# Kernel optimization log

Measured on AMD Instinct MI355X. Metric: run time of the kernel, lower is better.

The kernel has to match this reference:

```python
import jax, jax.numpy as jnp
import numpy as np

T = 16384
D_IN = 512
D_HID = 512
D_OUT = 512


def setup_inputs() -> dict:
    key = jax.random.key(0)
    ks = jax.random.split(key, 7)
    s_in = 1.0 / np.sqrt(D_IN)
    s_hid = 1.0 / np.sqrt(D_HID)
    xs = jax.random.normal(ks[0], (T, D_IN), dtype=jnp.float32)
    Wz = jax.random.uniform(ks[1], (D_HID, D_IN), jnp.float32, -s_in, s_in)
    bz = jax.random.uniform(ks[2], (D_HID,), jnp.float32, -s_in, s_in)
    Wh = jax.random.uniform(ks[3], (D_HID, D_IN), jnp.float32, -s_in, s_in)
    bh = jax.random.uniform(ks[4], (D_HID,), jnp.float32, -s_in, s_in)
    Wo = jax.random.uniform(ks[5], (D_OUT, D_HID), jnp.float32, -s_hid, s_hid)
    bo = jax.random.uniform(ks[6], (D_OUT,), jnp.float32, -s_hid, s_hid)
    return {"xs": xs, "Wz": Wz, "bz": bz, "Wh": Wh, "bh": bh, "Wo": Wo, "bo": bo}


def _combine(first, second):
    a0, b0 = first
    a1, b1 = second
    return (a0 * a1, a1 * b0 + b1)


def reference(xs, Wz, bz, Wh, bh, Wo, bo):
    # gates and candidate hidden states: [T, H]
    zs = jax.nn.sigmoid(xs @ Wz.T + bz)
    hs = xs @ Wh.T + bh
    # prepend identity element (a=1, b=0) for the h_0 = 0 initial state
    a = jnp.concatenate([jnp.ones((1, zs.shape[1]), zs.dtype), 1.0 - zs], axis=0)
    b = jnp.concatenate([jnp.zeros((1, zs.shape[1]), zs.dtype), zs * hs], axis=0)
    _, states = jax.lax.associative_scan(_combine, (a, b))  # [T+1, H]
    return states[1:] @ Wo.T + bo  # [T, D_OUT]
```

## Files before the change

kernel.cpp:

```cpp
#include <hip/hip_runtime.h>
#include <hip/hip_bf16.h>
#include <cstdint>
#include <cmath>

#define T_SEQ 16384
#define DMODEL 512
#define NCHUNK 512
#define LCHUNK 32
#define W_N    (DMODEL * DMODEL)
#define N4_W   (W_N / 4)
#define N4_W3  (3 * N4_W)
#define N4_X   (T_SEQ * DMODEL / 4)
#define N4_ALL (N4_W3 + N4_X)
#define NTILE  8

typedef __bf16 bf16x8 __attribute__((ext_vector_type(8)));
typedef float  f32x4  __attribute__((ext_vector_type(4)));

using bf16 = __hip_bfloat16;

__device__ __forceinline__ void load_lds16(const void* g, void* l) {
    __builtin_amdgcn_global_load_lds((const __attribute__((address_space(1))) void*)g,
                                     (__attribute__((address_space(3))) void*)l,
                                     16, 0, 0);
}

__device__ __forceinline__ unsigned short f2bf(float f) {
    union { float f; unsigned u; } v; v.f = f;
    const unsigned r = (v.u + 0x7FFFu + ((v.u >> 16) & 1u)) >> 16;
    return (unsigned short)r;
}
__device__ __forceinline__ float bf2f(unsigned short u) {
    union { unsigned u; float f; } v; v.u = ((unsigned)u) << 16;
    return v.f;
}

__device__ __forceinline__ void comb(float& A, float& B, float fA, float fB,
                                     float sA, float sB) {
    A = fA * sA;
    B = sA * fB + sB;
}

__global__ __launch_bounds__(256) void k_convert(
    const float* __restrict__ xs,
    const float* __restrict__ Wz, const float* __restrict__ Wh,
    const float* __restrict__ Wo,
    bf16* __restrict__ xs_c, bf16* __restrict__ Wz_c,
    bf16* __restrict__ Wh_c, bf16* __restrict__ Wo_c)
{
    const int i = blockIdx.x * 256 + threadIdx.x;
    if (i >= N4_ALL) return;
    const float* src; bf16* dst; int o;
    if (i < N4_W3) {
        const int w = i >> 16; o = i & 65535;
        src = (w == 0) ? Wz : (w == 1) ? Wh : Wo;
        dst = (w == 0) ? Wz_c : (w == 1) ? Wh_c : Wo_c;
    } else {
        o = i - N4_W3; src = xs; dst = xs_c;
    }
    const float4 v = ((const float4*)src)[o];
    ushort4 r;
    r.x = f2bf(v.x); r.y = f2bf(v.y); r.z = f2bf(v.z); r.w = f2bf(v.w);
    ((ushort4*)dst)[o] = r;
}

__global__ __launch_bounds__(512, 2) void gemm_zh(
    const bf16* __restrict__ xs_c, const bf16* __restrict__ Wz, const float* __restrict__ bz,
    const bf16* __restrict__ Wh, const float* __restrict__ bh,
    unsigned int* __restrict__ ab_ws,
    float* __restrict__ AaggT, float* __restrict__ BaggT)
{
    __shared__ __bf16 As[2][2][256 * 32];
    __shared__ __bf16 Zs[2][2][128 * 32];
    __shared__ __bf16 Hs[2][2][128 * 32];

    const int tid  = threadIdx.x;
    const int bm   = blockIdx.x;
    const int bn   = blockIdx.y;
    const int lane = tid & 63;
    const int wave = tid >> 6;
    const int wm   = wave >> 1;
    const int wn   = wave & 1;
    const int quad = lane >> 4;
    const int col  = lane & 15;

    f32x4 accz[4][4], acch[4][4];
    #pragma unroll
    for (int i = 0; i < 4; ++i)
        #pragma unroll
        for (int j = 0; j < 4; ++j) {
            accz[i][j] = (f32x4){0.f, 0.f, 0.f, 0.f};
            acch[i][j] = (f32x4){0.f, 0.f, 0.f, 0.f};
        }

    const int srow = tid >> 2;
    const int wq   = (tid & 3) ^ ((tid >> 3) & 3);
    const bf16* ag = xs_c + (size_t)(bm * 256 + srow) * DMODEL + wq * 8;
    const bf16* zg = Wz   + (size_t)(bn * 128 + srow) * DMODEL + wq * 8;
    const bf16* hg = Wh   + (size_t)(bn * 128 + srow) * DMODEL + wq * 8;

    const int fq = quad ^ ((col >> 1) & 3);
    int offA[4], offB[4];
    #pragma unroll
    for (int i = 0; i < 4; ++i) {
        offA[i] = (wm * 64 + i * 16 + col) * 32 + fq * 8;
        offB[i] = (wn * 64 + i * 16 + col) * 32 + fq * 8;
    }

    auto STAGE_HALF = [&](int t, int h) {
        const int b  = t & 1;
        const int ko = t * 64 + h * 32;
        load_lds16(ag + ko,                          &As[b][h][tid * 8]);
        load_lds16(ag + (size_t)128 * DMODEL + ko,   &As[b][h][(512 + tid) * 8]);
        load_lds16(zg + ko,                          &Zs[b][h][tid * 8]);
        load_lds16(hg + ko,                          &Hs[b][h][tid * 8]);
    };

    STAGE_HALF(0, 0); STAGE_HALF(0, 1);

    #pragma unroll
    for (int t = 0; t < NTILE; ++t) {
        const int b = t & 1;
        bf16x8 af[4], zf[4], hf[4];

        asm volatile("s_waitcnt vmcnt(4)" ::: "memory");
        __builtin_amdgcn_s_barrier();
        __builtin_amdgcn_sched_barrier(0);
        if (t + 1 < NTILE) STAGE_HALF(t + 1, 0);
        #pragma unroll
        for (int i = 0; i < 4; ++i) {
            af[i] = *(const bf16x8*)&As[b][0][offA[i]];
            zf[i] = *(const bf16x8*)&Zs[b][0][offB[i]];
        }
        __builtin_amdgcn_s_setprio(1);
        #pragma unroll
        for (int i = 0; i < 4; ++i)
            #pragma unroll
            for (int j = 0; j < 4; ++j)
                accz[i][j] = __builtin_amdgcn_mfma_f32_16x16x32_bf16(af[i], zf[j], accz[i][j], 0, 0, 0);
        __builtin_amdgcn_s_setprio(0);

        #pragma unroll
        for (int j = 0; j < 4; ++j)
            hf[j] = *(const bf16x8*)&Hs[b][0][offB[j]];
        __builtin_amdgcn_s_setprio(1);
        #pragma unroll
        for (int i = 0; i < 4; ++i)
            #pragma unroll
            for (int j = 0; j < 4; ++j)
                acch[i][j] = __builtin_amdgcn_mfma_f32_16x16x32_bf16(af[i], hf[j], acch[i][j], 0, 0, 0);
        __builtin_amdgcn_s_setprio(0);

        if (t + 1 < NTILE) {
            asm volatile("s_waitcnt vmcnt(4)" ::: "memory");
        } else {
            asm volatile("s_waitcnt vmcnt(0)" ::: "memory");
        }
        __builtin_amdgcn_s_barrier();
        __builtin_amdgcn_sched_barrier(0);
        if (t + 1 < NTILE) STAGE_HALF(t + 1, 1);
        #pragma unroll
        for (int i = 0; i < 4; ++i) {
            af[i] = *(const bf16x8*)&As[b][1][offA[i]];
            zf[i] = *(const bf16x8*)&Zs[b][1][offB[i]];
        }
        __builtin_amdgcn_s_setprio(1);
        #pragma unroll
        for (int i = 0; i < 4; ++i)
            #pragma unroll
            for (int j = 0; j < 4; ++j)
                accz[i][j] = __builtin_amdgcn_mfma_f32_16x16x32_bf16(af[i], zf[j], accz[i][j], 0, 0, 0);
        __builtin_amdgcn_s_setprio(0);

        #pragma unroll
        for (int j = 0; j < 4; ++j)
            hf[j] = *(const bf16x8*)&Hs[b][1][offB[j]];
        __builtin_amdgcn_s_setprio(1);
        #pragma unroll
        for (int i = 0; i < 4; ++i)
            #pragma unroll
            for (int j = 0; j < 4; ++j)
                acch[i][j] = __builtin_amdgcn_mfma_f32_16x16x32_bf16(af[i], hf[j], acch[i][j], 0, 0, 0);
        __builtin_amdgcn_s_setprio(0);
    }

    const int c_lo = bm * 8 + wm * 2;
    #pragma unroll
    for (int j = 0; j < 4; ++j) {
        const int n = bn * 128 + wn * 64 + j * 16 + col;
        const float bzv = bz[n];
        const float bhv = bh[n];
        float cA[4], cB[4];
        #pragma unroll
        for (int i = 0; i < 4; ++i) {
            const int mbase = bm * 256 + wm * 64 + i * 16 + quad * 4;
            float A = 1.f, B = 0.f;
            #pragma unroll
            for (int r = 0; r < 4; ++r) {
                const float zpre = accz[i][j][r] + bzv;
                const float hpre = acch[i][j][r] + bhv;
                const float z = 1.f / (1.f + __expf(-zpre));
                const float a = 1.f - z;
                const float b = z * hpre;
                const size_t idx = (size_t)(mbase + r) * DMODEL + n;
                ab_ws[idx] = (unsigned)f2bf(a) | ((unsigned)f2bf(b) << 16);
                A = a * A;
                B = a * B + b;
            }
            cA[i] = A; cB[i] = B;
        }
        #pragma unroll
        for (int i = 0; i < 4; ++i) {
            float pA = __shfl_xor(cA[i], 16);
            float pB = __shfl_xor(cB[i], 16);
            const bool hi1 = quad & 1;
            comb(cA[i], cB[i], hi1 ? pA : cA[i], hi1 ? pB : cB[i],
                               hi1 ? cA[i] : pA, hi1 ? cB[i] : pB);
            pA = __shfl_xor(cA[i], 32);
            pB = __shfl_xor(cB[i], 32);
            const bool hi2 = quad >> 1;
            comb(cA[i], cB[i], hi2 ? pA : cA[i], hi2 ? pB : cB[i],
                               hi2 ? cA[i] : pA, hi2 ? cB[i] : pB);
        }
        float Alo, Blo, Ahi, Bhi;
        comb(Alo, Blo, cA[0], cB[0], cA[1], cB[1]);
        comb(Ahi, Bhi, cA[2], cB[2], cA[3], cB[3]);
        if (quad == 0) {
            AaggT[(size_t)n * NCHUNK + c_lo]     = Alo;
            BaggT[(size_t)n * NCHUNK + c_lo]     = Blo;
            AaggT[(size_t)n * NCHUNK + c_lo + 1] = Ahi;
            BaggT[(size_t)n * NCHUNK + c_lo + 1] = Bhi;
        }
    }
}

__global__ __launch_bounds__(512) void scan_p2(
    const float* __restrict__ AaggT, const float* __restrict__ BaggT,
    float* __restrict__ HpreT)
{
    const int h = blockIdx.x;
    const int c = threadIdx.x;
    __shared__ float sA[NCHUNK], sB[NCHUNK];

    float A = AaggT[(size_t)h * NCHUNK + c];
    float B = BaggT[(size_t)h * NCHUNK + c];
    sA[c] = A; sB[c] = B;
    __syncthreads();

    for (int off = 1; off < NCHUNK; off <<= 1) {
        float pA = 1.f, pB = 0.f;
        if (c >= off) { pA = sA[c - off]; pB = sB[c - off]; }
        __syncthreads();
        const float nB = A * pB + B;
        const float nA = A * pA;
        A = nA; B = nB;
        sA[c] = A; sB[c] = B;
        __syncthreads();
    }
    const float hp = (c == 0) ? 0.f : sB[c - 1];
    HpreT[(size_t)h * NCHUNK + c] = hp;
}

__global__ __launch_bounds__(256) void scan_p3(
    const unsigned int* __restrict__ ab_ws, const float* __restrict__ HpreT,
    unsigned short* __restrict__ states)
{
    const int tid = threadIdx.x;
    const int c   = blockIdx.x;
    const int ch  = blockIdx.y * 256 + tid;
    float H = HpreT[(size_t)ch * NCHUNK + c];
    const size_t base = (size_t)(c * LCHUNK) * DMODEL + ch;
    #pragma unroll 8
    for (int i = 0; i < LCHUNK; ++i) {
        const unsigned u = ab_ws[base + (size_t)i * DMODEL];
        const float a = bf2f((unsigned short)(u & 0xFFFFu));
        const float b = bf2f((unsigned short)(u >> 16));
        H = a * H + b;
        states[base + (size_t)i * DMODEL] = f2bf(H);
    }
}

__global__ __launch_bounds__(512, 2) void gemm_out(
    const bf16* __restrict__ states, const bf16* __restrict__ Wo, const float* __restrict__ bo,
    float* __restrict__ out)
{
    __shared__ __bf16 As[2][2][256 * 32];
    __shared__ __bf16 Bs[2][2][128 * 32];

    const int tid  = threadIdx.x;
    const int bm   = blockIdx.x;
    const int bn   = blockIdx.y;
    const int lane = tid & 63;
    const int wave = tid >> 6;
    const int wm   = wave >> 1;
    const int wn   = wave & 1;
    const int quad = lane >> 4;
    const int col  = lane & 15;

    f32x4 acc[4][4];
    #pragma unroll
    for (int i = 0; i < 4; ++i)
        #pragma unroll
        for (int j = 0; j < 4; ++j)
            acc[i][j] = (f32x4){0.f, 0.f, 0.f, 0.f};

    const int srow = tid >> 2;
    const int wq   = (tid & 3) ^ ((tid >> 3) & 3);
    const bf16* ag = states + (size_t)(bm * 256 + srow) * DMODEL + wq * 8;
    const bf16* bg = Wo     + (size_t)(bn * 128 + srow) * DMODEL + wq * 8;

    const int fq = quad ^ ((col >> 1) & 3);
    int offA[4], offB[4];
    #pragma unroll
    for (int i = 0; i < 4; ++i) {
        offA[i] = (wm * 64 + i * 16 + col) * 32 + fq * 8;
        offB[i] = (wn * 64 + i * 16 + col) * 32 + fq * 8;
    }

    auto STAGE_HALF = [&](int t, int h) {
        const int b  = t & 1;
        const int ko = t * 64 + h * 32;
        load_lds16(ag + ko,                        &As[b][h][tid * 8]);
        load_lds16(ag + (size_t)128 * DMODEL + ko, &As[b][h][(512 + tid) * 8]);
        load_lds16(bg + ko,                        &Bs[b][h][tid * 8]);
    };

    STAGE_HALF(0, 0); STAGE_HALF(0, 1);

    #pragma unroll
    for (int t = 0; t < NTILE; ++t) {
        const int b = t & 1;
        bf16x8 af[4], bf[4];

        asm volatile("s_waitcnt vmcnt(3)" ::: "memory");
        __builtin_amdgcn_s_barrier();
        __builtin_amdgcn_sched_barrier(0);
        if (t + 1 < NTILE) STAGE_HALF(t + 1, 0);
        #pragma unroll
        for (int i = 0; i < 4; ++i) {
            af[i] = *(const bf16x8*)&As[b][0][offA[i]];
            bf[i] = *(const bf16x8*)&Bs[b][0][offB[i]];
        }
        __builtin_amdgcn_s_setprio(1);
        #pragma unroll
        for (int i = 0; i < 4; ++i)
            #pragma unroll
            for (int j = 0; j < 4; ++j)
                acc[i][j] = __builtin_amdgcn_mfma_f32_16x16x32_bf16(af[i], bf[j], acc[i][j], 0, 0, 0);
        __builtin_amdgcn_s_setprio(0);

        if (t + 1 < NTILE) {
            asm volatile("s_waitcnt vmcnt(3)" ::: "memory");
        } else {
            asm volatile("s_waitcnt vmcnt(0)" ::: "memory");
        }
        __builtin_amdgcn_s_barrier();
        __builtin_amdgcn_sched_barrier(0);
        if (t + 1 < NTILE) STAGE_HALF(t + 1, 1);
        #pragma unroll
        for (int i = 0; i < 4; ++i) {
            af[i] = *(const bf16x8*)&As[b][1][offA[i]];
            bf[i] = *(const bf16x8*)&Bs[b][1][offB[i]];
        }
        __builtin_amdgcn_s_setprio(1);
        #pragma unroll
        for (int i = 0; i < 4; ++i)
            #pragma unroll
            for (int j = 0; j < 4; ++j)
                acc[i][j] = __builtin_amdgcn_mfma_f32_16x16x32_bf16(af[i], bf[j], acc[i][j], 0, 0, 0);
        __builtin_amdgcn_s_setprio(0);
    }

    #pragma unroll
    for (int j = 0; j < 4; ++j) {
        const int n = bn * 128 + wn * 64 + j * 16 + col;
        const float bov = bo[n];
        #pragma unroll
        for (int i = 0; i < 4; ++i) {
            const int mbase = bm * 256 + wm * 64 + i * 16 + quad * 4;
            #pragma unroll
            for (int r = 0; r < 4; ++r)
                out[(size_t)(mbase + r) * DMODEL + n] = acc[i][j][r] + bov;
        }
    }
}

extern "C" void kernel_launch(void* const* d_in, const int* in_sizes, int n_in,
                              void* d_out, int out_size, void* d_ws, size_t ws_size,
                              hipStream_t stream)
{
    const float* xs = (const float*)d_in[0];
    const float* Wz = (const float*)d_in[1];
    const float* bz = (const float*)d_in[2];
    const float* Wh = (const float*)d_in[3];
    const float* bh = (const float*)d_in[4];
    const float* Wo = (const float*)d_in[5];
    const float* bo = (const float*)d_in[6];
    float* out = (float*)d_out;

    char* w = (char*)d_ws;
    bf16*  Wz_c   = (bf16*) (w);
    bf16*  Wh_c   = (bf16*) (w + 524288ull);
    bf16*  Wo_c   = (bf16*) (w + 1048576ull);
    unsigned int*   ab_ws  = (unsigned int*)  (w + 1572864ull);
    unsigned short* states = (unsigned short*)(w + 35127296ull);
    float* AaggT  = (float*)(w + 51904512ull);
    float* BaggT  = (float*)(w + 52953088ull);
    float* HpreT  = (float*)(w + 54001664ull);
    bf16*  xs_c   = (bf16*) states;

    k_convert<<<(N4_ALL + 255) / 256, 256, 0, stream>>>(xs, Wz, Wh, Wo, xs_c, Wz_c, Wh_c, Wo_c);
    gemm_zh<<<dim3(64, 4), 512, 0, stream>>>(xs_c, Wz_c, bz, Wh_c, bh, ab_ws, AaggT, BaggT);
    scan_p2<<<DMODEL, NCHUNK, 0, stream>>>(AaggT, BaggT, HpreT);
    scan_p3<<<dim3(NCHUNK, 2), 256, 0, stream>>>(ab_ws, HpreT, states);
    gemm_out<<<dim3(64, 4), 512, 0, stream>>>((const bf16*)states, Wo_c, bo, out);
}
```

Before: 150.2 us.

## Fuse fp32-to-bf16 conversion into GEMM loads and drop convert kernel

Removes the separate conversion kernel and instead has both GEMMs load fp32 inputs and weights through registers, convert them to bf16 and write them into LDS. This saves one kernel launch and the extra round trip through memory for the converted xs and weights. The price is dropping direct global-to-LDS loads, halving the LDS buffering (one buffer per half instead of two), and making every block re-convert the weights. Global loads are now issued into registers one half-step ahead, which overlaps less latency than before.

New measurement: 172.9 us. +15.1%, slower.

```diff
diff --git a/kernel.cpp b/kernel.cpp
--- a/kernel.cpp
+++ b/kernel.cpp
@@ -7,23 +7,12 @@
 #define DMODEL 512
 #define NCHUNK 512
 #define LCHUNK 32
-#define W_N    (DMODEL * DMODEL)
-#define N4_W   (W_N / 4)
-#define N4_W3  (3 * N4_W)
-#define N4_X   (T_SEQ * DMODEL / 4)
-#define N4_ALL (N4_W3 + N4_X)
 #define NTILE  8
 
 typedef __bf16 bf16x8 __attribute__((ext_vector_type(8)));
 typedef float  f32x4  __attribute__((ext_vector_type(4)));
 
 using bf16 = __hip_bfloat16;
-
-__device__ __forceinline__ void load_lds16(const void* g, void* l) {
-    __builtin_amdgcn_global_load_lds((const __attribute__((address_space(1))) void*)g,
-                                     (__attribute__((address_space(3))) void*)l,
-                                     16, 0, 0);
-}
 
 __device__ __forceinline__ unsigned short f2bf(float f) {
     union { float f; unsigned u; } v; v.f = f;
@@ -34,6 +23,16 @@
     union { unsigned u; float f; } v; v.u = ((unsigned)u) << 16;
     return v.f;
 }
+__device__ __forceinline__ uint4 pack8(const float4 a, const float4 b) {
+    __hip_bfloat162 p0 = __float22bfloat162_rn(make_float2(a.x, a.y));
+    __hip_bfloat162 p1 = __float22bfloat162_rn(make_float2(a.z, a.w));
+    __hip_bfloat162 p2 = __float22bfloat162_rn(make_float2(b.x, b.y));
+    __hip_bfloat162 p3 = __float22bfloat162_rn(make_float2(b.z, b.w));
+    uint4 r;
+    r.x = *(const unsigned*)&p0; r.y = *(const unsigned*)&p1;
+    r.z = *(const unsigned*)&p2; r.w = *(const unsigned*)&p3;
+    return r;
+}
 
 __device__ __forceinline__ void comb(float& A, float& B, float fA, float fB,
                                      float sA, float sB) {
@@ -41,38 +40,15 @@
     B = sA * fB + sB;
 }
 
-__global__ __launch_bounds__(256) void k_convert(
-    const float* __restrict__ xs,
-    const float* __restrict__ Wz, const float* __restrict__ Wh,
-    const float* __restrict__ Wo,
-    bf16* __restrict__ xs_c, bf16* __restrict__ Wz_c,
-    bf16* __restrict__ Wh_c, bf16* __restrict__ Wo_c)
-{
-    const int i = blockIdx.x * 256 + threadIdx.x;
-    if (i >= N4_ALL) return;
-    const float* src; bf16* dst; int o;
-    if (i < N4_W3) {
-        const int w = i >> 16; o = i & 65535;
-        src = (w == 0) ? Wz : (w == 1) ? Wh : Wo;
-        dst = (w == 0) ? Wz_c : (w == 1) ? Wh_c : Wo_c;
-    } else {
-        o = i - N4_W3; src = xs; dst = xs_c;
-    }
-    const float4 v = ((const float4*)src)[o];
-    ushort4 r;
-    r.x = f2bf(v.x); r.y = f2bf(v.y); r.z = f2bf(v.z); r.w = f2bf(v.w);
-    ((ushort4*)dst)[o] = r;
-}
-
-__global__ __launch_bounds__(512, 2) void gemm_zh(
-    const bf16* __restrict__ xs_c, const bf16* __restrict__ Wz, const float* __restrict__ bz,
-    const bf16* __restrict__ Wh, const float* __restrict__ bh,
+__global__ __launch_bounds__(512) void gemm_zh(
+    const float* __restrict__ xs, const float* __restrict__ Wz, const float* __restrict__ bz,
+    const float* __restrict__ Wh, const float* __restrict__ bh,
     unsigned int* __restrict__ ab_ws,
     float* __restrict__ AaggT, float* __restrict__ BaggT)
 {
-    __shared__ __bf16 As[2][2][256 * 32];
-    __shared__ __bf16 Zs[2][2][128 * 32];
-    __shared__ __bf16 Hs[2][2][128 * 32];
+    __shared__ __bf16 As[2][256 * 32];
+    __shared__ __bf16 Zs[2][128 * 32];
+    __shared__ __bf16 Hs[2][128 * 32];
 
     const int tid  = threadIdx.x;
     const int bm   = blockIdx.x;
@@ -93,11 +69,17 @@
             acch[i][j] = (f32x4){0.f, 0.f, 0.f, 0.f};
         }
 
-    const int srow = tid >> 2;
-    const int wq   = (tid & 3) ^ ((tid >> 3) & 3);
-    const bf16* ag = xs_c + (size_t)(bm * 256 + srow) * DMODEL + wq * 8;
-    const bf16* zg = Wz   + (size_t)(bn * 128 + srow) * DMODEL + wq * 8;
-    const bf16* hg = Wh   + (size_t)(bn * 128 + srow) * DMODEL + wq * 8;
+    const int arow = tid >> 1;
+    const int as0  = (tid & 1) * 2;
+    const float* xg = xs + (size_t)(bm * 256 + arow) * DMODEL + (tid & 1) * 16;
+    const int asw   = (arow >> 1) & 3;
+    const int aoff0 = arow * 32 + ((as0    ) ^ asw) * 8;
+    const int aoff1 = arow * 32 + ((as0 + 1) ^ asw) * 8;
+
+    const int wrow = tid >> 2;
+    const float* zg = Wz + (size_t)(bn * 128 + wrow) * DMODEL + (tid & 3) * 8;
+    const float* hg = Wh + (size_t)(bn * 128 + wrow) * DMODEL + (tid & 3) * 8;
+    const int woff = wrow * 32 + ((tid & 3) ^ ((wrow >> 1) & 3)) * 8;
 
     const int fq = quad ^ ((col >> 1) & 3);
     int offA[4], offB[4];
@@ -107,30 +89,37 @@
         offB[i] = (wn * 64 + i * 16 + col) * 32 + fq * 8;
     }
 
-    auto STAGE_HALF = [&](int t, int h) {
-        const int b  = t & 1;
+    float4 xa[4], za[2], ha[2];
+    auto XLOAD = [&](int t, int h) {
         const int ko = t * 64 + h * 32;
-        load_lds16(ag + ko,                          &As[b][h][tid * 8]);
-        load_lds16(ag + (size_t)128 * DMODEL + ko,   &As[b][h][(512 + tid) * 8]);
-        load_lds16(zg + ko,                          &Zs[b][h][tid * 8]);
-        load_lds16(hg + ko,                          &Hs[b][h][tid * 8]);
+        #pragma unroll
+        for (int f = 0; f < 4; ++f)
+            xa[f] = *(const float4*)(xg + ko + f * 4);
+        za[0] = *(const float4*)(zg + ko); za[1] = *(const float4*)(zg + ko + 4);
+        ha[0] = *(const float4*)(hg + ko); ha[1] = *(const float4*)(hg + ko + 4);
     };
-
-    STAGE_HALF(0, 0); STAGE_HALF(0, 1);
+    auto XWRITE = [&](int h) {
+        *(uint4*)&As[h][aoff0] = pack8(xa[0], xa[1]);
+        *(uint4*)&As[h][aoff1] = pack8(xa[2], xa[3]);
+        *(uint4*)&Zs[h][woff]  = pack8(za[0], za[1]);
+        *(uint4*)&Hs[h][woff]  = pack8(ha[0], ha[1]);
+    };
+
+    XLOAD(0, 0);
 
     #pragma unroll
     for (int t = 0; t < NTILE; ++t) {
-        const int b = t & 1;
         bf16x8 af[4], zf[4], hf[4];
 
-        asm volatile("s_waitcnt vmcnt(4)" ::: "memory");
+        XWRITE(0);
+        asm volatile("s_waitcnt lgkmcnt(0)" ::: "memory");
         __builtin_amdgcn_s_barrier();
         __builtin_amdgcn_sched_barrier(0);
-        if (t + 1 < NTILE) STAGE_HALF(t + 1, 0);
-        #pragma unroll
-        for (int i = 0; i < 4; ++i) {
-            af[i] = *(const bf16x8*)&As[b][0][offA[i]];
-            zf[i] = *(const bf16x8*)&Zs[b][0][offB[i]];
+        XLOAD(t, 1);
+        #pragma unroll
+        for (int i = 0; i < 4; ++i) {
+            af[i] = *(const bf16x8*)&As[0][offA[i]];
+            zf[i] = *(const bf16x8*)&Zs[0][offB[i]];
         }
         __builtin_amdgcn_s_setprio(1);
         #pragma unroll
@@ -142,7 +131,7 @@
 
         #pragma unroll
         for (int j = 0; j < 4; ++j)
-            hf[j] = *(const bf16x8*)&Hs[b][0][offB[j]];
+            hf[j] = *(const bf16x8*)&Hs[0][offB[j]];
         __builtin_amdgcn_s_setprio(1);
         #pragma unroll
         for (int i = 0; i < 4; ++i)
@@ -151,18 +140,15 @@
                 acch[i][j] = __builtin_amdgcn_mfma_f32_16x16x32_bf16(af[i], hf[j], acch[i][j], 0, 0, 0);
         __builtin_amdgcn_s_setprio(0);
 
-        if (t + 1 < NTILE) {
-            asm volatile("s_waitcnt vmcnt(4)" ::: "memory");
-        } else {
-            asm volatile("s_waitcnt vmcnt(0)" ::: "memory");
-        }
+        XWRITE(1);
+        asm volatile("s_waitcnt lgkmcnt(0)" ::: "memory");
         __builtin_amdgcn_s_barrier();
         __builtin_amdgcn_sched_barrier(0);
-        if (t + 1 < NTILE) STAGE_HALF(t + 1, 1);
-        #pragma unroll
-        for (int i = 0; i < 4; ++i) {
-            af[i] = *(const bf16x8*)&As[b][1][offA[i]];
-            zf[i] = *(const bf16x8*)&Zs[b][1][offB[i]];
+        if (t + 1 < NTILE) XLOAD(t + 1, 0);
+        #pragma unroll
+        for (int i = 0; i < 4; ++i) {
+            af[i] = *(const bf16x8*)&As[1][offA[i]];
+            zf[i] = *(const bf16x8*)&Zs[1][offB[i]];
         }
         __builtin_amdgcn_s_setprio(1);
         #pragma unroll
@@ -174,7 +160,7 @@
 
         #pragma unroll
         for (int j = 0; j < 4; ++j)
-            hf[j] = *(const bf16x8*)&Hs[b][1][offB[j]];
+            hf[j] = *(const bf16x8*)&Hs[1][offB[j]];
         __builtin_amdgcn_s_setprio(1);
         #pragma unroll
         for (int i = 0; i < 4; ++i)
@@ -280,12 +266,12 @@
     }
 }
 
-__global__ __launch_bounds__(512, 2) void gemm_out(
-    const bf16* __restrict__ states, const bf16* __restrict__ Wo, const float* __restrict__ bo,
-    float* __restrict__ out)
+__global__ __launch_bounds__(512) void gemm_out(
+    const unsigned short* __restrict__ states, const float* __restrict__ Wo,
+    const float* __restrict__ bo, float* __restrict__ out)
 {
-    __shared__ __bf16 As[2][2][256 * 32];
-    __shared__ __bf16 Bs[2][2][128 * 32];
+    __shared__ __bf16 As[2][256 * 32];
+    __shared__ __bf16 Bs[2][128 * 32];
 
     const int tid  = threadIdx.x;
     const int bm   = blockIdx.x;
@@ -304,10 +290,16 @@
         for (int j = 0; j < 4; ++j)
             acc[i][j] = (f32x4){0.f, 0.f, 0.f, 0.f};
 
-    const int srow = tid >> 2;
-    const int wq   = (tid & 3) ^ ((tid >> 3) & 3);
-    const bf16* ag = states + (size_t)(bm * 256 + srow) * DMODEL + wq * 8;
-    const bf16* bg = Wo     + (size_t)(bn * 128 + srow) * DMODEL + wq * 8;
+    const int arow = tid >> 1;
+    const int as0  = (tid & 1) * 2;
+    const unsigned short* ag = states + (size_t)(bm * 256 + arow) * DMODEL + (tid & 1) * 16;
+    const int asw   = (arow >> 1) & 3;
+    const int aoff0 = arow * 32 + ((as0    ) ^ asw) * 8;
+    const int aoff1 = arow * 32 + ((as0 + 1) ^ asw) * 8;
+
+    const int wrow = tid >> 2;
+    const float* bg = Wo + (size_t)(bn * 128 + wrow) * DMODEL + (tid & 3) * 8;
+    const int woff = wrow * 32 + ((tid & 3) ^ ((wrow >> 1) & 3)) * 8;
 
     const int fq = quad ^ ((col >> 1) & 3);
     int offA[4], offB[4];
@@ -317,29 +309,40 @@
         offB[i] = (wn * 64 + i * 16 + col) * 32 + fq * 8;
     }
 
-    auto STAGE_HALF = [&](int t, int h) {
-        const int b  = t & 1;
-        const int ko = t * 64 + h * 32;
-        load_lds16(ag + ko,                        &As[b][h][tid * 8]);
-        load_lds16(ag + (size_t)128 * DMODEL + ko, &As[b][h][(512 + tid) * 8]);
-        load_lds16(bg + ko,                        &Bs[b][h][tid * 8]);
+    uint4  xa0[2], xa1[2];
+    float4 wb0[2], wb1[2];
+    auto XLOAD0 = [&](int t) {
+        const int ko = t * 64;
+        xa0[0] = *(const uint4*)(ag + ko);
+        xa0[1] = *(const uint4*)(ag + ko + 8);
+        wb0[0] = *(const float4*)(bg + ko);
+        wb0[1] = *(const float4*)(bg + ko + 4);
     };
-
-    STAGE_HALF(0, 0); STAGE_HALF(0, 1);
+    auto XLOAD1 = [&](int t) {
+        const int ko = t * 64 + 32;
+        xa1[0] = *(const uint4*)(ag + ko);
+        xa1[1] = *(const uint4*)(ag + ko + 8);
+        wb1[0] = *(const float4*)(bg + ko);
+        wb1[1] = *(const float4*)(bg + ko + 4);
+    };
+
+    XLOAD0(0); XLOAD1(0);
 
     #pragma unroll
     for (int t = 0; t < NTILE; ++t) {
-        const int b = t & 1;
         bf16x8 af[4], bf[4];
 
-        asm volatile("s_waitcnt vmcnt(3)" ::: "memory");
+        *(uint4*)&As[0][aoff0] = xa0[0];
+        *(uint4*)&As[0][aoff1] = xa0[1];
+        *(uint4*)&Bs[0][woff]  = pack8(wb0[0], wb0[1]);
+        asm volatile("s_waitcnt lgkmcnt(0)" ::: "memory");
         __builtin_amdgcn_s_barrier();
         __builtin_amdgcn_sched_barrier(0);
-        if (t + 1 < NTILE) STAGE_HALF(t + 1, 0);
-        #pragma unroll
-        for (int i = 0; i < 4; ++i) {
-            af[i] = *(const bf16x8*)&As[b][0][offA[i]];
-            bf[i] = *(const bf16x8*)&Bs[b][0][offB[i]];
+        if (t + 1 < NTILE) XLOAD0(t + 1);
+        #pragma unroll
+        for (int i = 0; i < 4; ++i) {
+            af[i] = *(const bf16x8*)&As[0][offA[i]];
+            bf[i] = *(const bf16x8*)&Bs[0][offB[i]];
         }
         __builtin_amdgcn_s_setprio(1);
         #pragma unroll
@@ -349,18 +352,17 @@
                 acc[i][j] = __builtin_amdgcn_mfma_f32_16x16x32_bf16(af[i], bf[j], acc[i][j], 0, 0, 0);
         __builtin_amdgcn_s_setprio(0);
 
-        if (t + 1 < NTILE) {
-            asm volatile("s_waitcnt vmcnt(3)" ::: "memory");
-        } else {
-            asm volatile("s_waitcnt vmcnt(0)" ::: "memory");
-        }
+        *(uint4*)&As[1][aoff0] = xa1[0];
+        *(uint4*)&As[1][aoff1] = xa1[1];
+        *(uint4*)&Bs[1][woff]  = pack8(wb1[0], wb1[1]);
+        asm volatile("s_waitcnt lgkmcnt(0)" ::: "memory");
         __builtin_amdgcn_s_barrier();
         __builtin_amdgcn_sched_barrier(0);
-        if (t + 1 < NTILE) STAGE_HALF(t + 1, 1);
-        #pragma unroll
-        for (int i = 0; i < 4; ++i) {
-            af[i] = *(const bf16x8*)&As[b][1][offA[i]];
-            bf[i] = *(const bf16x8*)&Bs[b][1][offB[i]];
+        if (t + 1 < NTILE) XLOAD1(t + 1);
+        #pragma unroll
+        for (int i = 0; i < 4; ++i) {
+            af[i] = *(const bf16x8*)&As[1][offA[i]];
+            bf[i] = *(const bf16x8*)&Bs[1][offB[i]];
         }
         __builtin_amdgcn_s_setprio(1);
         #pragma unroll
@@ -399,19 +401,14 @@
     float* out = (float*)d_out;
 
     char* w = (char*)d_ws;
-    bf16*  Wz_c   = (bf16*) (w);
-    bf16*  Wh_c   = (bf16*) (w + 524288ull);
-    bf16*  Wo_c   = (bf16*) (w + 1048576ull);
-    unsigned int*   ab_ws  = (unsigned int*)  (w + 1572864ull);
-    unsigned short* states = (unsigned short*)(w + 35127296ull);
-    float* AaggT  = (float*)(w + 51904512ull);
-    float* BaggT  = (float*)(w + 52953088ull);
-    float* HpreT  = (float*)(w + 54001664ull);
-    bf16*  xs_c   = (bf16*) states;
-
-    k_convert<<<(N4_ALL + 255) / 256, 256, 0, stream>>>(xs, Wz, Wh, Wo, xs_c, Wz_c, Wh_c, Wo_c);
-    gemm_zh<<<dim3(64, 4), 512, 0, stream>>>(xs_c, Wz_c, bz, Wh_c, bh, ab_ws, AaggT, BaggT);
+    unsigned int*   ab_ws  = (unsigned int*)  (w);
+    unsigned short* states = (unsigned short*)(w + 33554432ull);
+    float* AaggT  = (float*)(w + 50331648ull);
+    float* BaggT  = (float*)(w + 51380224ull);
+    float* HpreT  = (float*)(w + 52428800ull);
+
+    gemm_zh<<<dim3(64, 4), 512, 0, stream>>>(xs, Wz, bz, Wh, bh, ab_ws, AaggT, BaggT);
     scan_p2<<<DMODEL, NCHUNK, 0, stream>>>(AaggT, BaggT, HpreT);
     scan_p3<<<dim3(NCHUNK, 2), 256, 0, stream>>>(ab_ws, HpreT, states);
-    gemm_out<<<dim3(64, 4), 512, 0, stream>>>((const bf16*)states, Wo_c, bo, out);
-}
+    gemm_out<<<dim3(64, 4), 512, 0, stream>>>(states, Wo, bo, out);
+}
```

## Fuse chunk-local scan replay with output GEMM and interleave A/B aggregates

Applied to the files above, without the earlier changes.

The chunk-local scan replay (scan_p3) and the output projection GEMM become one kernel. Each block handles one 32-step chunk, writes its bf16 states straight into swizzled LDS, and multiplies them by the full Wo, streamed through a triple-buffered LDS pipeline. This removes the global round trip of the states tensor and one kernel launch. The cost is that every block reloads all of Wo (512 blocks times 512 KB, mostly served from L2) and works on a small 32-row M tile, which lowers MFMA reuse per Wo load. The A and B chunk aggregates are also interleaved into a single float2 array, so the scan writes and reads them with vector accesses.

After: 153.3 us. 1.02x slower.

```diff
diff --git a/kernel.cpp b/kernel.cpp
--- a/kernel.cpp
+++ b/kernel.cpp
@@ -13,6 +13,7 @@
 #define N4_X   (T_SEQ * DMODEL / 4)
 #define N4_ALL (N4_W3 + N4_X)
 #define NTILE  8
+#define NHALF  16
 
 typedef __bf16 bf16x8 __attribute__((ext_vector_type(8)));
 typedef float  f32x4  __attribute__((ext_vector_type(4)));
@@ -68,7 +69,7 @@
     const bf16* __restrict__ xs_c, const bf16* __restrict__ Wz, const float* __restrict__ bz,
     const bf16* __restrict__ Wh, const float* __restrict__ bh,
     unsigned int* __restrict__ ab_ws,
-    float* __restrict__ AaggT, float* __restrict__ BaggT)
+    float* __restrict__ ABagg)
 {
     __shared__ __bf16 As[2][2][256 * 32];
     __shared__ __bf16 Zs[2][2][128 * 32];
@@ -226,24 +227,22 @@
         comb(Alo, Blo, cA[0], cB[0], cA[1], cB[1]);
         comb(Ahi, Bhi, cA[2], cB[2], cA[3], cB[3]);
         if (quad == 0) {
-            AaggT[(size_t)n * NCHUNK + c_lo]     = Alo;
-            BaggT[(size_t)n * NCHUNK + c_lo]     = Blo;
-            AaggT[(size_t)n * NCHUNK + c_lo + 1] = Ahi;
-            BaggT[(size_t)n * NCHUNK + c_lo + 1] = Bhi;
+            *(float4*)&ABagg[((size_t)n * NCHUNK + c_lo) * 2] =
+                make_float4(Alo, Blo, Ahi, Bhi);
         }
     }
 }
 
 __global__ __launch_bounds__(512) void scan_p2(
-    const float* __restrict__ AaggT, const float* __restrict__ BaggT,
-    float* __restrict__ HpreT)
+    const float* __restrict__ ABagg, float* __restrict__ HpreT)
 {
     const int h = blockIdx.x;
     const int c = threadIdx.x;
     __shared__ float sA[NCHUNK], sB[NCHUNK];
 
-    float A = AaggT[(size_t)h * NCHUNK + c];
-    float B = BaggT[(size_t)h * NCHUNK + c];
+    const float2 v = ((const float2*)ABagg)[(size_t)h * NCHUNK + c];
+    float A = v.x;
+    float B = v.y;
     sA[c] = A; sB[c] = B;
     __syncthreads();
 
@@ -261,123 +260,103 @@
     HpreT[(size_t)h * NCHUNK + c] = hp;
 }
 
-__global__ __launch_bounds__(256) void scan_p3(
+__global__ __launch_bounds__(512) void fused_p3o(
     const unsigned int* __restrict__ ab_ws, const float* __restrict__ HpreT,
-    unsigned short* __restrict__ states)
-{
-    const int tid = threadIdx.x;
-    const int c   = blockIdx.x;
-    const int ch  = blockIdx.y * 256 + tid;
-    float H = HpreT[(size_t)ch * NCHUNK + c];
-    const size_t base = (size_t)(c * LCHUNK) * DMODEL + ch;
-    #pragma unroll 8
-    for (int i = 0; i < LCHUNK; ++i) {
-        const unsigned u = ab_ws[base + (size_t)i * DMODEL];
-        const float a = bf2f((unsigned short)(u & 0xFFFFu));
-        const float b = bf2f((unsigned short)(u >> 16));
-        H = a * H + b;
-        states[base + (size_t)i * DMODEL] = f2bf(H);
-    }
-}
-
-__global__ __launch_bounds__(512, 2) void gemm_out(
-    const bf16* __restrict__ states, const bf16* __restrict__ Wo, const float* __restrict__ bo,
+    const bf16* __restrict__ Wo, const float* __restrict__ bo,
     float* __restrict__ out)
 {
-    __shared__ __bf16 As[2][2][256 * 32];
-    __shared__ __bf16 Bs[2][2][128 * 32];
+    __shared__ __bf16 Ss[32 * 512];
+    __shared__ __bf16 Ws[3][512 * 32];
 
     const int tid  = threadIdx.x;
-    const int bm   = blockIdx.x;
-    const int bn   = blockIdx.y;
+    const int c    = blockIdx.x;
     const int lane = tid & 63;
     const int wave = tid >> 6;
-    const int wm   = wave >> 1;
-    const int wn   = wave & 1;
     const int quad = lane >> 4;
     const int col  = lane & 15;
 
-    f32x4 acc[4][4];
-    #pragma unroll
-    for (int i = 0; i < 4; ++i)
+    const int row0 = tid >> 2;
+    const int wq   = (tid & 3) ^ ((tid >> 3) & 3);
+    const bf16* bg = Wo + (size_t)row0 * DMODEL + wq * 8;
+
+    auto STAGE = [&](int h, int p) {
+        const int ko = h * 32;
+        #pragma unroll
+        for (int it = 0; it < 4; ++it)
+            load_lds16(bg + (size_t)(it * 128) * DMODEL + ko,
+                       &Ws[p][(it * 512 + tid) * 8]);
+    };
+
+    STAGE(0, 0); STAGE(1, 1);
+
+    {
+        float H = HpreT[(size_t)tid * NCHUNK + c];
+        const size_t base = (size_t)(c * LCHUNK) * DMODEL + tid;
+        const int sslot = tid >> 3;
+        const int selem = tid & 7;
+        #pragma unroll 8
+        for (int i = 0; i < LCHUNK; ++i) {
+            const unsigned u = ab_ws[base + (size_t)i * DMODEL];
+            const float a = bf2f((unsigned short)(u & 0xFFFFu));
+            const float b = bf2f((unsigned short)(u >> 16));
+            H = a * H + b;
+            const int ps = sslot ^ (i & 7);
+            *(unsigned short*)&Ss[i * 512 + ps * 8 + selem] = f2bf(H);
+        }
+    }
+    __syncthreads();
+
+    f32x4 acc[2][4];
+    #pragma unroll
+    for (int i = 0; i < 2; ++i)
         #pragma unroll
         for (int j = 0; j < 4; ++j)
             acc[i][j] = (f32x4){0.f, 0.f, 0.f, 0.f};
 
-    const int srow = tid >> 2;
-    const int wq   = (tid & 3) ^ ((tid >> 3) & 3);
-    const bf16* ag = states + (size_t)(bm * 256 + srow) * DMODEL + wq * 8;
-    const bf16* bg = Wo     + (size_t)(bn * 128 + srow) * DMODEL + wq * 8;
-
-    const int fq = quad ^ ((col >> 1) & 3);
-    int offA[4], offB[4];
-    #pragma unroll
-    for (int i = 0; i < 4; ++i) {
-        offA[i] = (wm * 64 + i * 16 + col) * 32 + fq * 8;
-        offB[i] = (wn * 64 + i * 16 + col) * 32 + fq * 8;
-    }
-
-    auto STAGE_HALF = [&](int t, int h) {
-        const int b  = t & 1;
-        const int ko = t * 64 + h * 32;
-        load_lds16(ag + ko,                        &As[b][h][tid * 8]);
-        load_lds16(ag + (size_t)128 * DMODEL + ko, &As[b][h][(512 + tid) * 8]);
-        load_lds16(bg + ko,                        &Bs[b][h][tid * 8]);
-    };
-
-    STAGE_HALF(0, 0); STAGE_HALF(0, 1);
-
-    #pragma unroll
-    for (int t = 0; t < NTILE; ++t) {
-        const int b = t & 1;
-        bf16x8 af[4], bf[4];
-
-        asm volatile("s_waitcnt vmcnt(3)" ::: "memory");
+    const int fq   = quad ^ ((col >> 1) & 3);
+    const int keyA = col & 7;
+    int offB[4];
+    #pragma unroll
+    for (int j = 0; j < 4; ++j)
+        offB[j] = (wave * 64 + j * 16 + col) * 32 + fq * 8;
+
+    for (int h = 0; h < NHALF; ++h) {
+        if (h + 1 < NHALF) {
+            asm volatile("s_waitcnt vmcnt(4)" ::: "memory");
+        } else {
+            asm volatile("s_waitcnt vmcnt(0)" ::: "memory");
+        }
         __builtin_amdgcn_s_barrier();
         __builtin_amdgcn_sched_barrier(0);
-        if (t + 1 < NTILE) STAGE_HALF(t + 1, 0);
-        #pragma unroll
-        for (int i = 0; i < 4; ++i) {
-            af[i] = *(const bf16x8*)&As[b][0][offA[i]];
-            bf[i] = *(const bf16x8*)&Bs[b][0][offB[i]];
-        }
-        __builtin_amdgcn_s_setprio(1);
-        #pragma unroll
-        for (int i = 0; i < 4; ++i)
+        if (h + 2 < NHALF) STAGE(h + 2, (h + 2) % 3);
+
+        const int p = h % 3;
+        bf16x8 af[2], bf[4];
+        #pragma unroll
+        for (int i = 0; i < 2; ++i) {
+            const int ps = ((h << 2) | quad) ^ keyA;
+            af[i] = *(const bf16x8*)&Ss[(i * 16 + col) * 512 + ps * 8];
+        }
+        #pragma unroll
+        for (int j = 0; j < 4; ++j)
+            bf[j] = *(const bf16x8*)&Ws[p][offB[j]];
+
+        __builtin_amdgcn_s_setprio(1);
+        #pragma unroll
+        for (int i = 0; i < 2; ++i)
             #pragma unroll
             for (int j = 0; j < 4; ++j)
                 acc[i][j] = __builtin_amdgcn_mfma_f32_16x16x32_bf16(af[i], bf[j], acc[i][j], 0, 0, 0);
         __builtin_amdgcn_s_setprio(0);
-
-        if (t + 1 < NTILE) {
-            asm volatile("s_waitcnt vmcnt(3)" ::: "memory");
-        } else {
-            asm volatile("s_waitcnt vmcnt(0)" ::: "memory");
-        }
-        __builtin_amdgcn_s_barrier();
-        __builtin_amdgcn_sched_barrier(0);
-        if (t + 1 < NTILE) STAGE_HALF(t + 1, 1);
-        #pragma unroll
-        for (int i = 0; i < 4; ++i) {
-            af[i] = *(const bf16x8*)&As[b][1][offA[i]];
-            bf[i] = *(const bf16x8*)&Bs[b][1][offB[i]];
-        }
-        __builtin_amdgcn_s_setprio(1);
-        #pragma unroll
-        for (int i = 0; i < 4; ++i)
-            #pragma unroll
-            for (int j = 0; j < 4; ++j)
-                acc[i][j] = __builtin_amdgcn_mfma_f32_16x16x32_bf16(af[i], bf[j], acc[i][j], 0, 0, 0);
-        __builtin_amdgcn_s_setprio(0);
     }
 
     #pragma unroll
     for (int j = 0; j < 4; ++j) {
-        const int n = bn * 128 + wn * 64 + j * 16 + col;
+        const int n = wave * 64 + j * 16 + col;
         const float bov = bo[n];
         #pragma unroll
-        for (int i = 0; i < 4; ++i) {
-            const int mbase = bm * 256 + wm * 64 + i * 16 + quad * 4;
+        for (int i = 0; i < 2; ++i) {
+            const int mbase = c * LCHUNK + i * 16 + quad * 4;
             #pragma unroll
             for (int r = 0; r < 4; ++r)
                 out[(size_t)(mbase + r) * DMODEL + n] = acc[i][j][r] + bov;
@@ -399,19 +378,16 @@
     float* out = (float*)d_out;
 
     char* w = (char*)d_ws;
-    bf16*  Wz_c   = (bf16*) (w);
-    bf16*  Wh_c   = (bf16*) (w + 524288ull);
-    bf16*  Wo_c   = (bf16*) (w + 1048576ull);
-    unsigned int*   ab_ws  = (unsigned int*)  (w + 1572864ull);
-    unsigned short* states = (unsigned short*)(w + 35127296ull);
-    float* AaggT  = (float*)(w + 51904512ull);
-    float* BaggT  = (float*)(w + 52953088ull);
+    unsigned int* ab_ws = (unsigned int*)(w);
+    bf16*  xs_c   = (bf16*) (w + 33554432ull);
+    bf16*  Wz_c   = (bf16*) (w + 50331648ull);
+    bf16*  Wh_c   = (bf16*) (w + 50855936ull);
+    bf16*  Wo_c   = (bf16*) (w + 51380224ull);
+    float* ABagg  = (float*)(w + 51904512ull);
     float* HpreT  = (float*)(w + 54001664ull);
-    bf16*  xs_c   = (bf16*) states;
 
     k_convert<<<(N4_ALL + 255) / 256, 256, 0, stream>>>(xs, Wz, Wh, Wo, xs_c, Wz_c, Wh_c, Wo_c);
-    gemm_zh<<<dim3(64, 4), 512, 0, stream>>>(xs_c, Wz_c, bz, Wh_c, bh, ab_ws, AaggT, BaggT);
-    scan_p2<<<DMODEL, NCHUNK, 0, stream>>>(AaggT, BaggT, HpreT);
-    scan_p3<<<dim3(NCHUNK, 2), 256, 0, stream>>>(ab_ws, HpreT, states);
-    gemm_out<<<dim3(64, 4), 512, 0, stream>>>((const bf16*)states, Wo_c, bo, out);
-}
+    gemm_zh<<<dim3(64, 4), 512, 0, stream>>>(xs_c, Wz_c, bz, Wh_c, bh, ab_ws, ABagg);
+    scan_p2<<<DMODEL, NCHUNK, 0, stream>>>(ABagg, HpreT);
+    fused_p3o<<<NCHUNK, 512, 0, stream>>>(ab_ws, HpreT, Wo_c, bo, out);
+}
```
